# Optimization experiments

Hardware: AMD Instinct MI355X
Metric: run time of the kernel (lower is better)

## Reference

```python
import jax, jax.numpy as jnp
import numpy as np

D_MODEL = 1024
D_K = 64
B, S = 4, 2048


def setup_inputs() -> dict:
    key = jax.random.key(0)
    k1, k2, k3, k4, k5, k6, k7 = jax.random.split(key, 7)
    return {
        "query": jax.random.normal(k1, (B, S, D_MODEL), dtype=jnp.float32),
        "key": jax.random.normal(k2, (B, S, D_MODEL), dtype=jnp.float32),
        "value": jax.random.normal(k3, (B, S, D_MODEL), dtype=jnp.float32),
        "mask": jax.random.randint(k4, (B, S, S), 0, 2).astype(jnp.bool_),
        # nn.Linear(d_model, d_k, bias=False) weights, stored as [d_k, d_model] like torch
        "w_q": jax.random.normal(k5, (D_K, D_MODEL), dtype=jnp.float32) * (D_MODEL ** -0.5),
        "w_k": jax.random.normal(k6, (D_K, D_MODEL), dtype=jnp.float32) * (D_MODEL ** -0.5),
        "w_v": jax.random.normal(k7, (D_K, D_MODEL), dtype=jnp.float32) * (D_MODEL ** -0.5),
    }


def reference(query, key, value, mask, w_q, w_k, w_v):
    # Linear projections (torch Linear: x @ W.T)
    q = jnp.einsum("bsm,km->bsk", query, w_q)   # [B,S,d_k]
    k = jnp.einsum("bsm,km->bsk", key, w_k)
    v = jnp.einsum("bsm,km->bsk", value, w_v)
    # NOTE: original scales by d_model**-0.5 (not d_k) — keep faithful.
    scores = jnp.einsum("bqk,bsk->bqs", q, k) * (D_MODEL ** -0.5)  # [B,S,S]
    # NOTE: original fills masked positions with 1e-9 (not -inf) BEFORE softmax.
    scores = jnp.where(mask, jnp.float32(1e-9), scores)
    probs = jax.nn.softmax(scores, axis=-1)
    return jnp.einsum("bqs,bsk->bqk", probs, v)  # [B,S,d_k]
```

## Files before the change

kernel.cpp:

```cpp
#include <hip/hip_runtime.h>

#define B_    4
#define S_    2048
#define DM_   1024
#define DK_   64
#define SCALE_ 0.03125f

typedef float        f32x4  __attribute__((ext_vector_type(4)));
typedef float        float8 __attribute__((ext_vector_type(8)));
typedef short        short8 __attribute__((ext_vector_type(8)));
typedef float        fltx4  __attribute__((ext_vector_type(4)));
typedef unsigned int uint2v __attribute__((ext_vector_type(2)));
typedef unsigned int uint4v __attribute__((ext_vector_type(4)));

static __device__ __forceinline__ unsigned short f2bf(float f) {
  unsigned u = __float_as_uint(f);
  u += 0x7fffu + ((u >> 16) & 1u);
  return (unsigned short)(u >> 16);
}
static __device__ __forceinline__ uint2v pack4(float a, float b, float c, float d) {
  uint2v r;
  r.x = (unsigned)f2bf(a) | ((unsigned)f2bf(b) << 16);
  r.y = (unsigned)f2bf(c) | ((unsigned)f2bf(d) << 16);
  return r;
}
static __device__ __forceinline__ short8 cvt8(float8 v) {
  short8 r;
#pragma unroll
  for (int i = 0; i < 8; ++i) r[i] = (short)f2bf(v[i]);
  return r;
}

__global__ void detect_kernel(const unsigned int* __restrict__ m, unsigned int* __restrict__ flag) {
  unsigned v = m[threadIdx.x];
  unsigned long long bad = __ballot(v > 1u);
  if (threadIdx.x == 0) flag[0] = (bad != 0ull) ? 1u : 0u;
}

__global__ __launch_bounds__(256) void wconv_kernel(
    const float* __restrict__ wq, const float* __restrict__ wk, const float* __restrict__ wv,
    unsigned short* __restrict__ Wb)
{
  const int idx   = blockIdx.x * 256 + threadIdx.x;
  const int which = idx >> 13;
  const int e     = idx & 8191;
  const float* __restrict__ w = (which == 0) ? wq : (which == 1) ? wk : wv;
  fltx4 v0 = *reinterpret_cast<const fltx4*>(w + (size_t)e * 8);
  fltx4 v1 = *reinterpret_cast<const fltx4*>(w + (size_t)e * 8 + 4);
  uint4v o;
  o.x = (unsigned)f2bf(v0.x) | ((unsigned)f2bf(v0.y) << 16);
  o.y = (unsigned)f2bf(v0.z) | ((unsigned)f2bf(v0.w) << 16);
  o.z = (unsigned)f2bf(v1.x) | ((unsigned)f2bf(v1.y) << 16);
  o.w = (unsigned)f2bf(v1.z) | ((unsigned)f2bf(v1.w) << 16);
  *reinterpret_cast<uint4v*>(Wb + (size_t)which * 65536 + (size_t)e * 8) = o;
}

__global__ __launch_bounds__(256) void maskpack_kernel(const unsigned char* __restrict__ mb,
                                                       const unsigned int* __restrict__ mi,
                                                       const unsigned int* __restrict__ flag,
                                                       unsigned int* __restrict__ mp) {
  const int w = blockIdx.x * 256 + threadIdx.x;
  unsigned out = 0;
  if (flag[0]) {
    const uint4v* p = reinterpret_cast<const uint4v*>(mb + (size_t)w * 32);
    uint4v a = p[0], b = p[1];
    unsigned ws0[8];
    ws0[0]=a.x; ws0[1]=a.y; ws0[2]=a.z; ws0[3]=a.w; ws0[4]=b.x; ws0[5]=b.y; ws0[6]=b.z; ws0[7]=b.w;
#pragma unroll
    for (int i = 0; i < 8; ++i) {
      unsigned v = ws0[i];
      out |= ((v & 0x000000ffu) ? 1u : 0u) << (i * 4 + 0);
      out |= ((v & 0x0000ff00u) ? 1u : 0u) << (i * 4 + 1);
      out |= ((v & 0x00ff0000u) ? 1u : 0u) << (i * 4 + 2);
      out |= ((v & 0xff000000u) ? 1u : 0u) << (i * 4 + 3);
    }
  } else {
    const uint4v* p = reinterpret_cast<const uint4v*>(mi + (size_t)w * 32);
#pragma unroll
    for (int i = 0; i < 8; ++i) {
      uint4v a = p[i];
      out |= (a.x ? 1u : 0u) << (i * 4 + 0);
      out |= (a.y ? 1u : 0u) << (i * 4 + 1);
      out |= (a.z ? 1u : 0u) << (i * 4 + 2);
      out |= (a.w ? 1u : 0u) << (i * 4 + 3);
    }
  }
  mp[w] = out;
}

__global__ __launch_bounds__(256) void proj3_kernel(
    const float* __restrict__ xq, const float* __restrict__ xk, const float* __restrict__ xv,
    const unsigned short* __restrict__ Wb,
    unsigned short* __restrict__ Qp, unsigned short* __restrict__ Kp, unsigned short* __restrict__ Vt)
{
  const int which = blockIdx.y;
  const float* __restrict__ x = (which == 0) ? xq : (which == 1) ? xk : xv;
  const int row0 = blockIdx.x * 16;
  const int tid = threadIdx.x, wid = tid >> 6, lane = tid & 63;
  const int g = lane >> 4, r16 = lane & 15;

  const float* __restrict__ xrow = x + (size_t)(row0 + r16) * DM_ + wid * 256 + g * 8;
  const unsigned short* __restrict__ wbase = Wb + (size_t)which * 65536 + wid * 256 + g * 8;

  f32x4 acc[4];
#pragma unroll
  for (int i = 0; i < 4; ++i) { acc[i].x = 0.f; acc[i].y = 0.f; acc[i].z = 0.f; acc[i].w = 0.f; }

#pragma unroll
  for (int kc = 0; kc < 8; ++kc) {
    float8 xa = *reinterpret_cast<const float8*>(xrow + kc * 32);
    short8 w0 = *reinterpret_cast<const short8*>(wbase + (size_t)(0 * 16 + r16) * DM_ + kc * 32);
    short8 w1 = *reinterpret_cast<const short8*>(wbase + (size_t)(1 * 16 + r16) * DM_ + kc * 32);
    short8 w2 = *reinterpret_cast<const short8*>(wbase + (size_t)(2 * 16 + r16) * DM_ + kc * 32);
    short8 w3 = *reinterpret_cast<const short8*>(wbase + (size_t)(3 * 16 + r16) * DM_ + kc * 32);
    short8 a = cvt8(xa);
    acc[0] = __builtin_amdgcn_mfma_f32_16x16x32_bf16(a, w0, acc[0], 0, 0, 0);
    acc[1] = __builtin_amdgcn_mfma_f32_16x16x32_bf16(a, w1, acc[1], 0, 0, 0);
    acc[2] = __builtin_amdgcn_mfma_f32_16x16x32_bf16(a, w2, acc[2], 0, 0, 0);
    acc[3] = __builtin_amdgcn_mfma_f32_16x16x32_bf16(a, w3, acc[3], 0, 0, 0);
  }

  __shared__ f32x4 red[4][4][64];
#pragma unroll
  for (int nf = 0; nf < 4; ++nf) red[wid][nf][lane] = acc[nf];
  __syncthreads();

  f32x4 s = red[0][wid][lane];
#pragma unroll
  for (int w = 1; w < 4; ++w) {
    f32x4 t = red[w][wid][lane];
    s.x += t.x; s.y += t.y; s.z += t.z; s.w += t.w;
  }

  if (which < 2) {
    unsigned short* __restrict__ dst = (which == 0) ? Qp : Kp;
#pragma unroll
    for (int j = 0; j < 4; ++j)
      dst[(size_t)(row0 + g * 4 + j) * DK_ + wid * 16 + r16] = f2bf(s[j]);
  } else {
    const int grow = row0 + g * 4;
    const int bb = grow >> 11, sin = grow & 2047;
    *reinterpret_cast<uint2v*>(Vt + (size_t)(bb * DK_ + wid * 16 + r16) * S_ + sin) =
        pack4(s.x, s.y, s.z, s.w);
  }
}

__global__ __launch_bounds__(64) void attn_part_kernel(
    const unsigned short* __restrict__ Qp, const unsigned short* __restrict__ Kp,
    const unsigned short* __restrict__ Vt, const unsigned int* __restrict__ mp,
    float* __restrict__ pacc, float* __restrict__ pm, float* __restrict__ pl)
{
  const int lane = threadIdx.x;
  const int g = lane >> 4, r16 = lane & 15;
  const int bx = blockIdx.x;
  const int sp = bx >> 9;
  const int qw = bx & 511;
  const int b  = qw >> 7;
  const int q0 = (qw & 127) * 16;

  __shared__ __align__(16) unsigned short Kt[64][72];
  __shared__ __align__(16) unsigned short Vs[64][72];
  __shared__ __align__(16) unsigned short Pq[16][72];

  short8 aq0, aq1;
  {
    const unsigned short* qrow = Qp + (size_t)(b * S_ + q0 + r16) * DK_ + g * 8;
    aq0 = *reinterpret_cast<const short8*>(qrow);
    aq1 = *reinterpret_cast<const short8*>(qrow + 32);
  }

  float mrun[4], lsum[4], corr[4];
  f32x4 acc[4];
#pragma unroll
  for (int j = 0; j < 4; ++j) { mrun[j] = -3.0e38f; lsum[j] = 0.f; }
#pragma unroll
  for (int nf = 0; nf < 4; ++nf) { acc[nf].x = 0.f; acc[nf].y = 0.f; acc[nf].z = 0.f; acc[nf].w = 0.f; }

  const int srow_stage = lane >> 3, sgran = lane & 7;

  for (int st = sp * 8; st < sp * 8 + 8; ++st) {
    const int s0 = st * 64;
#pragma unroll
    for (int i = 0; i < 8; ++i) {
      int r = i * 8 + srow_stage;
      uint4v kv = *reinterpret_cast<const uint4v*>(Kp + (size_t)(b * S_ + s0 + r) * DK_ + sgran * 8);
      *reinterpret_cast<uint4v*>(&Kt[r][sgran * 8]) = kv;
      uint4v vv = *reinterpret_cast<const uint4v*>(Vt + (size_t)(b * DK_ + r) * S_ + s0 + sgran * 8);
      *reinterpret_cast<uint4v*>(&Vs[r][sgran * 8]) = vv;
    }
    unsigned long long mw[4];
#pragma unroll
    for (int j = 0; j < 4; ++j) {
      size_t widx = ((size_t)(b * S_ + q0 + g * 4 + j) * S_ + s0) >> 5;
      mw[j] = *reinterpret_cast<const unsigned long long*>(mp + widx);
    }
    __syncthreads();

    f32x4 sc[4];
#pragma unroll
    for (int nf = 0; nf < 4; ++nf) { sc[nf].x = 0.f; sc[nf].y = 0.f; sc[nf].z = 0.f; sc[nf].w = 0.f; }
#pragma unroll
    for (int nf = 0; nf < 4; ++nf) {
      short8 bk0 = *reinterpret_cast<const short8*>(&Kt[nf * 16 + r16][g * 8]);
      short8 bk1 = *reinterpret_cast<const short8*>(&Kt[nf * 16 + r16][32 + g * 8]);
      sc[nf] = __builtin_amdgcn_mfma_f32_16x16x32_bf16(aq0, bk0, sc[nf], 0, 0, 0);
      sc[nf] = __builtin_amdgcn_mfma_f32_16x16x32_bf16(aq1, bk1, sc[nf], 0, 0, 0);
    }
#pragma unroll
    for (int nf = 0; nf < 4; ++nf)
#pragma unroll
      for (int j = 0; j < 4; ++j) {
        float v = sc[nf][j] * SCALE_;
        sc[nf][j] = ((mw[j] >> (nf * 16 + r16)) & 1ull) ? 1e-9f : v;
      }
#pragma unroll
    for (int j = 0; j < 4; ++j) {
      float tm = fmaxf(fmaxf(sc[0][j], sc[1][j]), fmaxf(sc[2][j], sc[3][j]));
#pragma unroll
      for (int off = 1; off < 16; off <<= 1) tm = fmaxf(tm, __shfl_xor(tm, off));
      float mn = fmaxf(mrun[j], tm);
      corr[j] = __expf(mrun[j] - mn);
      mrun[j] = mn;
    }
#pragma unroll
    for (int nf = 0; nf < 4; ++nf)
#pragma unroll
      for (int j = 0; j < 4; ++j)
        sc[nf][j] = __expf(sc[nf][j] - mrun[j]);
#pragma unroll
    for (int j = 0; j < 4; ++j) {
      float rs = (sc[0][j] + sc[1][j]) + (sc[2][j] + sc[3][j]);
#pragma unroll
      for (int off = 1; off < 16; off <<= 1) rs += __shfl_xor(rs, off);
      lsum[j] = lsum[j] * corr[j] + rs;
    }
#pragma unroll
    for (int nf = 0; nf < 4; ++nf) {
      acc[nf].x *= corr[0]; acc[nf].y *= corr[1]; acc[nf].z *= corr[2]; acc[nf].w *= corr[3];
    }
#pragma unroll
    for (int nf = 0; nf < 4; ++nf)
#pragma unroll
      for (int j = 0; j < 4; ++j)
        Pq[g * 4 + j][nf * 16 + r16] = f2bf(sc[nf][j]);
    asm volatile("s_waitcnt lgkmcnt(0)" ::: "memory");

#pragma unroll
    for (int k2 = 0; k2 < 2; ++k2) {
      short8 pa = *reinterpret_cast<const short8*>(&Pq[r16][k2 * 32 + g * 8]);
#pragma unroll
      for (int nf = 0; nf < 4; ++nf) {
        short8 bv = *reinterpret_cast<const short8*>(&Vs[nf * 16 + r16][k2 * 32 + g * 8]);
        acc[nf] = __builtin_amdgcn_mfma_f32_16x16x32_bf16(pa, bv, acc[nf], 0, 0, 0);
      }
    }
    __syncthreads();
  }

  float* __restrict__ pa = pacc + (size_t)(sp * 512 + qw) * 1024;
#pragma unroll
  for (int nf = 0; nf < 4; ++nf)
#pragma unroll
    for (int j = 0; j < 4; ++j)
      pa[(g * 4 + j) * 64 + nf * 16 + r16] = acc[nf][j];
  if (r16 == 0) {
#pragma unroll
    for (int j = 0; j < 4; ++j) {
      pm[(sp * 512 + qw) * 16 + g * 4 + j] = mrun[j];
      pl[(sp * 512 + qw) * 16 + g * 4 + j] = lsum[j];
    }
  }
}

__global__ __launch_bounds__(64) void attn_merge_kernel(
    const float* __restrict__ pacc, const float* __restrict__ pm, const float* __restrict__ pl,
    float* __restrict__ out)
{
  const int qw = blockIdx.x;
  const int b = qw >> 7, q0 = (qw & 127) * 16;
  const int lane = threadIdx.x;

#pragma unroll 1
  for (int row = 0; row < 16; ++row) {
    float m0 = pm[(0 * 512 + qw) * 16 + row], m1 = pm[(1 * 512 + qw) * 16 + row];
    float m2 = pm[(2 * 512 + qw) * 16 + row], m3 = pm[(3 * 512 + qw) * 16 + row];
    float M = fmaxf(fmaxf(m0, m1), fmaxf(m2, m3));
    float w0 = __expf(m0 - M), w1 = __expf(m1 - M), w2 = __expf(m2 - M), w3 = __expf(m3 - M);
    float L = w0 * pl[(0 * 512 + qw) * 16 + row] + w1 * pl[(1 * 512 + qw) * 16 + row] +
              w2 * pl[(2 * 512 + qw) * 16 + row] + w3 * pl[(3 * 512 + qw) * 16 + row];
    float v = w0 * pacc[((size_t)(0 * 512 + qw) * 16 + row) * 64 + lane] +
              w1 * pacc[((size_t)(1 * 512 + qw) * 16 + row) * 64 + lane] +
              w2 * pacc[((size_t)(2 * 512 + qw) * 16 + row) * 64 + lane] +
              w3 * pacc[((size_t)(3 * 512 + qw) * 16 + row) * 64 + lane];
    out[(size_t)(b * S_ + q0 + row) * DK_ + lane] = v / L;
  }
}

__global__ __launch_bounds__(64) void attn_kernel(
    const unsigned short* __restrict__ Qp, const unsigned short* __restrict__ Kp,
    const unsigned short* __restrict__ Vt, const unsigned int* __restrict__ mp,
    float* __restrict__ out)
{
  const int lane = threadIdx.x;
  const int g = lane >> 4, r16 = lane & 15;
  const int qt = blockIdx.x & 127;
  const int b  = blockIdx.x >> 7;
  const int q0 = qt * 16;

  __shared__ __align__(16) unsigned short Kt[64][72];
  __shared__ __align__(16) unsigned short Vs[64][72];
  __shared__ __align__(16) unsigned short Pq[16][72];

  short8 aq0, aq1;
  {
    const unsigned short* qrow = Qp + (size_t)(b * S_ + q0 + r16) * DK_ + g * 8;
    aq0 = *reinterpret_cast<const short8*>(qrow);
    aq1 = *reinterpret_cast<const short8*>(qrow + 32);
  }

  float mrun[4], lsum[4], corr[4];
  f32x4 acc[4];
#pragma unroll
  for (int j = 0; j < 4; ++j) { mrun[j] = -3.0e38f; lsum[j] = 0.f; }
#pragma unroll
  for (int nf = 0; nf < 4; ++nf) { acc[nf].x = 0.f; acc[nf].y = 0.f; acc[nf].z = 0.f; acc[nf].w = 0.f; }

  const int srow_stage = lane >> 3, sgran = lane & 7;

  for (int st = 0; st < 32; ++st) {
    const int s0 = st * 64;
#pragma unroll
    for (int i = 0; i < 8; ++i) {
      int r = i * 8 + srow_stage;
      uint4v kv = *reinterpret_cast<const uint4v*>(Kp + (size_t)(b * S_ + s0 + r) * DK_ + sgran * 8);
      *reinterpret_cast<uint4v*>(&Kt[r][sgran * 8]) = kv;
      uint4v vv = *reinterpret_cast<const uint4v*>(Vt + (size_t)(b * DK_ + r) * S_ + s0 + sgran * 8);
      *reinterpret_cast<uint4v*>(&Vs[r][sgran * 8]) = vv;
    }
    unsigned long long mw[4];
#pragma unroll
    for (int j = 0; j < 4; ++j) {
      size_t widx = ((size_t)(b * S_ + q0 + g * 4 + j) * S_ + s0) >> 5;
      mw[j] = *reinterpret_cast<const unsigned long long*>(mp + widx);
    }
    __syncthreads();

    f32x4 sc[4];
#pragma unroll
    for (int nf = 0; nf < 4; ++nf) { sc[nf].x = 0.f; sc[nf].y = 0.f; sc[nf].z = 0.f; sc[nf].w = 0.f; }
#pragma unroll
    for (int nf = 0; nf < 4; ++nf) {
      short8 bk0 = *reinterpret_cast<const short8*>(&Kt[nf * 16 + r16][g * 8]);
      short8 bk1 = *reinterpret_cast<const short8*>(&Kt[nf * 16 + r16][32 + g * 8]);
      sc[nf] = __builtin_amdgcn_mfma_f32_16x16x32_bf16(aq0, bk0, sc[nf], 0, 0, 0);
      sc[nf] = __builtin_amdgcn_mfma_f32_16x16x32_bf16(aq1, bk1, sc[nf], 0, 0, 0);
    }
#pragma unroll
    for (int nf = 0; nf < 4; ++nf)
#pragma unroll
      for (int j = 0; j < 4; ++j) {
        float v = sc[nf][j] * SCALE_;
        sc[nf][j] = ((mw[j] >> (nf * 16 + r16)) & 1ull) ? 1e-9f : v;
      }
#pragma unroll
    for (int j = 0; j < 4; ++j) {
      float tm = fmaxf(fmaxf(sc[0][j], sc[1][j]), fmaxf(sc[2][j], sc[3][j]));
#pragma unroll
      for (int off = 1; off < 16; off <<= 1) tm = fmaxf(tm, __shfl_xor(tm, off));
      float mn = fmaxf(mrun[j], tm);
      corr[j] = __expf(mrun[j] - mn);
      mrun[j] = mn;
    }
#pragma unroll
    for (int nf = 0; nf < 4; ++nf)
#pragma unroll
      for (int j = 0; j < 4; ++j)
        sc[nf][j] = __expf(sc[nf][j] - mrun[j]);
#pragma unroll
    for (int j = 0; j < 4; ++j) {
      float rs = (sc[0][j] + sc[1][j]) + (sc[2][j] + sc[3][j]);
#pragma unroll
      for (int off = 1; off < 16; off <<= 1) rs += __shfl_xor(rs, off);
      lsum[j] = lsum[j] * corr[j] + rs;
    }
#pragma unroll
    for (int nf = 0; nf < 4; ++nf) {
      acc[nf].x *= corr[0]; acc[nf].y *= corr[1]; acc[nf].z *= corr[2]; acc[nf].w *= corr[3];
    }
#pragma unroll
    for (int nf = 0; nf < 4; ++nf)
#pragma unroll
      for (int j = 0; j < 4; ++j)
        Pq[g * 4 + j][nf * 16 + r16] = f2bf(sc[nf][j]);
    asm volatile("s_waitcnt lgkmcnt(0)" ::: "memory");

#pragma unroll
    for (int k2 = 0; k2 < 2; ++k2) {
      short8 pa = *reinterpret_cast<const short8*>(&Pq[r16][k2 * 32 + g * 8]);
#pragma unroll
      for (int nf = 0; nf < 4; ++nf) {
        short8 bv = *reinterpret_cast<const short8*>(&Vs[nf * 16 + r16][k2 * 32 + g * 8]);
        acc[nf] = __builtin_amdgcn_mfma_f32_16x16x32_bf16(pa, bv, acc[nf], 0, 0, 0);
      }
    }
    __syncthreads();
  }

#pragma unroll
  for (int nf = 0; nf < 4; ++nf)
#pragma unroll
    for (int j = 0; j < 4; ++j)
      out[(size_t)(b * S_ + q0 + g * 4 + j) * DK_ + nf * 16 + r16] = acc[nf][j] / lsum[j];
}

extern "C" void kernel_launch(void* const* d_in, const int* in_sizes, int n_in,
                              void* d_out, int out_size, void* d_ws, size_t ws_size,
                              hipStream_t stream) {
  const float* q  = (const float*)d_in[0];
  const float* k  = (const float*)d_in[1];
  const float* v  = (const float*)d_in[2];
  const void*  mk = d_in[3];
  const float* wq = (const float*)d_in[4];
  const float* wk = (const float*)d_in[5];
  const float* wv = (const float*)d_in[6];

  char* ws = (char*)d_ws;
  unsigned short* Qp   = (unsigned short*)(ws);
  unsigned short* Kp   = (unsigned short*)(ws + (1u << 20));
  unsigned short* Vt   = (unsigned short*)(ws + (2u << 20));
  unsigned int*   mp   = (unsigned int*)  (ws + (3u << 20));
  unsigned int*   flag = (unsigned int*)  (ws + (5u << 20));
  unsigned short* Wb   = (unsigned short*)(ws + (5u << 20) + 4096);
  float*          pacc = (float*)(ws + (6u << 20));
  float*          pm   = (float*)(ws + (14u << 20));
  float*          pl   = (float*)(ws + (14u << 20) + (1u << 17));

  wconv_kernel<<<96, 256, 0, stream>>>(wq, wk, wv, Wb);
  detect_kernel<<<1, 64, 0, stream>>>((const unsigned int*)mk, flag);
  maskpack_kernel<<<2048, 256, 0, stream>>>((const unsigned char*)mk, (const unsigned int*)mk, flag, mp);
  proj3_kernel<<<dim3(512, 3), 256, 0, stream>>>(q, k, v, Wb, Qp, Kp, Vt);

  if (ws_size >= (15u << 20)) {
    attn_part_kernel<<<2048, 64, 0, stream>>>(Qp, Kp, Vt, mp, pacc, pm, pl);
    attn_merge_kernel<<<512, 64, 0, stream>>>(pacc, pm, pl, (float*)d_out);
  } else {
    attn_kernel<<<512, 64, 0, stream>>>(Qp, Kp, Vt, mp, (float*)d_out);
  }
}
```

Measured before the change: 98.61 us.

## Restructure projection kernel with 64-row tiles staged in LDS via direct global loads

The projection kernel now processes 64 rows per block instead of 16. X and weight tiles are loaded with global_load_lds into XOR-swizzled shared memory, and each wave owns 16 rows across the full K dimension, which removes the cross-wave split-K reduction. Each weight tile is now reused across four times more rows, but there are 4x fewer blocks (384) and two syncs per K step with no double buffering, so load latency is not overlapped.

Result: faster. 86.96 us (-11.8%).

```diff
diff --git a/kernel.cpp b/kernel.cpp
--- a/kernel.cpp
+++ b/kernel.cpp
@@ -13,6 +13,11 @@
 typedef unsigned int uint2v __attribute__((ext_vector_type(2)));
 typedef unsigned int uint4v __attribute__((ext_vector_type(4)));
 
+#define GLL16(gsrc, ldst)                                                   \
+  __builtin_amdgcn_global_load_lds(                                         \
+      (const __attribute__((address_space(1))) void*)(gsrc),                \
+      (__attribute__((address_space(3))) void*)(ldst), 16, 0, 0)
+
 static __device__ __forceinline__ unsigned short f2bf(float f) {
   unsigned u = __float_as_uint(f);
   u += 0x7fffu + ((u >> 16) & 1u);
@@ -22,12 +27,6 @@
   uint2v r;
   r.x = (unsigned)f2bf(a) | ((unsigned)f2bf(b) << 16);
   r.y = (unsigned)f2bf(c) | ((unsigned)f2bf(d) << 16);
-  return r;
-}
-static __device__ __forceinline__ short8 cvt8(float8 v) {
-  short8 r;
-#pragma unroll
-  for (int i = 0; i < 8; ++i) r[i] = (short)f2bf(v[i]);
   return r;
 }
 
@@ -88,60 +87,91 @@
   mp[w] = out;
 }
 
-__global__ __launch_bounds__(256) void proj3_kernel(
+__global__ __launch_bounds__(256) void proj4_kernel(
     const float* __restrict__ xq, const float* __restrict__ xk, const float* __restrict__ xv,
     const unsigned short* __restrict__ Wb,
     unsigned short* __restrict__ Qp, unsigned short* __restrict__ Kp, unsigned short* __restrict__ Vt)
 {
   const int which = blockIdx.y;
   const float* __restrict__ x = (which == 0) ? xq : (which == 1) ? xk : xv;
-  const int row0 = blockIdx.x * 16;
-  const int tid = threadIdx.x, wid = tid >> 6, lane = tid & 63;
-  const int g = lane >> 4, r16 = lane & 15;
-
-  const float* __restrict__ xrow = x + (size_t)(row0 + r16) * DM_ + wid * 256 + g * 8;
-  const unsigned short* __restrict__ wbase = Wb + (size_t)which * 65536 + wid * 256 + g * 8;
+  const unsigned short* __restrict__ wsrc = Wb + (size_t)which * 65536;
+  const int row0 = blockIdx.x * 64;
+  const int tid = threadIdx.x, wid = tid >> 6;
+  const int lane = tid & 63, g = lane >> 4, r16 = lane & 15;
+
+  __shared__ __align__(16) float          XsF[8192];
+  __shared__ __align__(16) unsigned short WsH[8192];
 
   f32x4 acc[4];
 #pragma unroll
   for (int i = 0; i < 4; ++i) { acc[i].x = 0.f; acc[i].y = 0.f; acc[i].z = 0.f; acc[i].w = 0.f; }
 
-#pragma unroll
-  for (int kc = 0; kc < 8; ++kc) {
-    float8 xa = *reinterpret_cast<const float8*>(xrow + kc * 32);
-    short8 w0 = *reinterpret_cast<const short8*>(wbase + (size_t)(0 * 16 + r16) * DM_ + kc * 32);
-    short8 w1 = *reinterpret_cast<const short8*>(wbase + (size_t)(1 * 16 + r16) * DM_ + kc * 32);
-    short8 w2 = *reinterpret_cast<const short8*>(wbase + (size_t)(2 * 16 + r16) * DM_ + kc * 32);
-    short8 w3 = *reinterpret_cast<const short8*>(wbase + (size_t)(3 * 16 + r16) * DM_ + kc * 32);
-    short8 a = cvt8(xa);
-    acc[0] = __builtin_amdgcn_mfma_f32_16x16x32_bf16(a, w0, acc[0], 0, 0, 0);
-    acc[1] = __builtin_amdgcn_mfma_f32_16x16x32_bf16(a, w1, acc[1], 0, 0, 0);
-    acc[2] = __builtin_amdgcn_mfma_f32_16x16x32_bf16(a, w2, acc[2], 0, 0, 0);
-    acc[3] = __builtin_amdgcn_mfma_f32_16x16x32_bf16(a, w3, acc[3], 0, 0, 0);
-  }
-
-  __shared__ f32x4 red[4][4][64];
-#pragma unroll
-  for (int nf = 0; nf < 4; ++nf) red[wid][nf][lane] = acc[nf];
-  __syncthreads();
-
-  f32x4 s = red[0][wid][lane];
-#pragma unroll
-  for (int w = 1; w < 4; ++w) {
-    f32x4 t = red[w][wid][lane];
-    s.x += t.x; s.y += t.y; s.z += t.z; s.w += t.w;
+  int xrow[8], xcol[8];
+#pragma unroll
+  for (int i = 0; i < 8; ++i) {
+    int L = i * 4096 + tid * 16;
+    int U = L ^ (((L >> 9) & 15) << 4);
+    xrow[i] = U >> 9;
+    xcol[i] = (U & 511) >> 2;
+  }
+  int wrow[4], wcol[4];
+#pragma unroll
+  for (int i = 0; i < 4; ++i) {
+    int L = i * 4096 + tid * 16;
+    int U = L ^ (((L >> 8) & 15) << 4);
+    wrow[i] = U >> 8;
+    wcol[i] = (U & 255) >> 1;
+  }
+
+  for (int kb = 0; kb < 8; ++kb) {
+    const int k0 = kb * 128;
+#pragma unroll
+    for (int i = 0; i < 8; ++i)
+      GLL16(x + (size_t)(row0 + xrow[i]) * DM_ + k0 + xcol[i],
+            (char*)XsF + i * 4096 + wid * 1024);
+#pragma unroll
+    for (int i = 0; i < 4; ++i)
+      GLL16(wsrc + (size_t)wrow[i] * DM_ + k0 + wcol[i],
+            (char*)WsH + i * 4096 + wid * 1024);
+    __syncthreads();
+
+#pragma unroll
+    for (int k2 = 0; k2 < 4; ++k2) {
+      const int la  = (wid * 16 + r16) * 512 + k2 * 128 + g * 32;
+      const int pa0 = la ^ (r16 << 4);
+      const int pa1 = (la + 16) ^ (r16 << 4);
+      fltx4 a0 = *reinterpret_cast<const fltx4*>((const char*)XsF + pa0);
+      fltx4 a1 = *reinterpret_cast<const fltx4*>((const char*)XsF + pa1);
+      short8 a;
+      a[0] = (short)f2bf(a0.x); a[1] = (short)f2bf(a0.y);
+      a[2] = (short)f2bf(a0.z); a[3] = (short)f2bf(a0.w);
+      a[4] = (short)f2bf(a1.x); a[5] = (short)f2bf(a1.y);
+      a[6] = (short)f2bf(a1.z); a[7] = (short)f2bf(a1.w);
+#pragma unroll
+      for (int nf = 0; nf < 4; ++nf) {
+        const int lb = (nf * 16 + r16) * 256 + k2 * 64 + g * 16;
+        const int pb = lb ^ (r16 << 4);
+        short8 b = *reinterpret_cast<const short8*>((const char*)WsH + pb);
+        acc[nf] = __builtin_amdgcn_mfma_f32_16x16x32_bf16(a, b, acc[nf], 0, 0, 0);
+      }
+    }
+    __syncthreads();
   }
 
   if (which < 2) {
     unsigned short* __restrict__ dst = (which == 0) ? Qp : Kp;
 #pragma unroll
-    for (int j = 0; j < 4; ++j)
-      dst[(size_t)(row0 + g * 4 + j) * DK_ + wid * 16 + r16] = f2bf(s[j]);
+    for (int nf = 0; nf < 4; ++nf)
+#pragma unroll
+      for (int j = 0; j < 4; ++j)
+        dst[(size_t)(row0 + wid * 16 + g * 4 + j) * DK_ + nf * 16 + r16] = f2bf(acc[nf][j]);
   } else {
-    const int grow = row0 + g * 4;
+    const int grow = row0 + wid * 16 + g * 4;
     const int bb = grow >> 11, sin = grow & 2047;
-    *reinterpret_cast<uint2v*>(Vt + (size_t)(bb * DK_ + wid * 16 + r16) * S_ + sin) =
-        pack4(s.x, s.y, s.z, s.w);
+#pragma unroll
+    for (int nf = 0; nf < 4; ++nf)
+      *reinterpret_cast<uint2v*>(Vt + (size_t)(bb * DK_ + nf * 16 + r16) * S_ + sin) =
+          pack4(acc[nf][0], acc[nf][1], acc[nf][2], acc[nf][3]);
   }
 }
 
@@ -438,7 +468,7 @@
   wconv_kernel<<<96, 256, 0, stream>>>(wq, wk, wv, Wb);
   detect_kernel<<<1, 64, 0, stream>>>((const unsigned int*)mk, flag);
   maskpack_kernel<<<2048, 256, 0, stream>>>((const unsigned char*)mk, (const unsigned int*)mk, flag, mp);
-  proj3_kernel<<<dim3(512, 3), 256, 0, stream>>>(q, k, v, Wb, Qp, Kp, Vt);
+  proj4_kernel<<<dim3(128, 3), 256, 0, stream>>>(q, k, v, Wb, Qp, Kp, Vt);
 
   if (ws_size >= (15u << 20)) {
     attn_part_kernel<<<2048, 64, 0, stream>>>(Qp, Kp, Vt, mp, pacc, pm, pl);
```

## Stage projection input rows in LDS as bf16 and split waves over output columns

Applied to the files above, without the earlier changes.

The projection kernel now loads each block's 16 input rows with coalesced float4 reads, converts them to bf16, and stores them in a 32 KB XOR-swizzled LDS tile. Each wave then computes one 16-column slice of the output over the full K dimension from LDS, so the cross-wave LDS reduction is gone. The aim is better global-load coalescing and no reduction step. The cost is a large LDS footprint that may limit occupancy, plus a longer serial chain of 32 MFMAs per wave.

New measurement: 96.01 us. 1.03x faster.

```diff
diff --git a/kernel.cpp b/kernel.cpp
--- a/kernel.cpp
+++ b/kernel.cpp
@@ -7,7 +7,6 @@
 #define SCALE_ 0.03125f
 
 typedef float        f32x4  __attribute__((ext_vector_type(4)));
-typedef float        float8 __attribute__((ext_vector_type(8)));
 typedef short        short8 __attribute__((ext_vector_type(8)));
 typedef float        fltx4  __attribute__((ext_vector_type(4)));
 typedef unsigned int uint2v __attribute__((ext_vector_type(2)));
@@ -22,12 +21,6 @@
   uint2v r;
   r.x = (unsigned)f2bf(a) | ((unsigned)f2bf(b) << 16);
   r.y = (unsigned)f2bf(c) | ((unsigned)f2bf(d) << 16);
-  return r;
-}
-static __device__ __forceinline__ short8 cvt8(float8 v) {
-  short8 r;
-#pragma unroll
-  for (int i = 0; i < 8; ++i) r[i] = (short)f2bf(v[i]);
   return r;
 }
 
@@ -88,7 +81,7 @@
   mp[w] = out;
 }
 
-__global__ __launch_bounds__(256) void proj3_kernel(
+__global__ __launch_bounds__(256) void proj12_kernel(
     const float* __restrict__ xq, const float* __restrict__ xk, const float* __restrict__ xv,
     const unsigned short* __restrict__ Wb,
     unsigned short* __restrict__ Qp, unsigned short* __restrict__ Kp, unsigned short* __restrict__ Vt)
@@ -96,52 +89,46 @@
   const int which = blockIdx.y;
   const float* __restrict__ x = (which == 0) ? xq : (which == 1) ? xk : xv;
   const int row0 = blockIdx.x * 16;
-  const int tid = threadIdx.x, wid = tid >> 6, lane = tid & 63;
-  const int g = lane >> 4, r16 = lane & 15;
-
-  const float* __restrict__ xrow = x + (size_t)(row0 + r16) * DM_ + wid * 256 + g * 8;
-  const unsigned short* __restrict__ wbase = Wb + (size_t)which * 65536 + wid * 256 + g * 8;
-
-  f32x4 acc[4];
-#pragma unroll
-  for (int i = 0; i < 4; ++i) { acc[i].x = 0.f; acc[i].y = 0.f; acc[i].z = 0.f; acc[i].w = 0.f; }
-
-#pragma unroll
-  for (int kc = 0; kc < 8; ++kc) {
-    float8 xa = *reinterpret_cast<const float8*>(xrow + kc * 32);
-    short8 w0 = *reinterpret_cast<const short8*>(wbase + (size_t)(0 * 16 + r16) * DM_ + kc * 32);
-    short8 w1 = *reinterpret_cast<const short8*>(wbase + (size_t)(1 * 16 + r16) * DM_ + kc * 32);
-    short8 w2 = *reinterpret_cast<const short8*>(wbase + (size_t)(2 * 16 + r16) * DM_ + kc * 32);
-    short8 w3 = *reinterpret_cast<const short8*>(wbase + (size_t)(3 * 16 + r16) * DM_ + kc * 32);
-    short8 a = cvt8(xa);
-    acc[0] = __builtin_amdgcn_mfma_f32_16x16x32_bf16(a, w0, acc[0], 0, 0, 0);
-    acc[1] = __builtin_amdgcn_mfma_f32_16x16x32_bf16(a, w1, acc[1], 0, 0, 0);
-    acc[2] = __builtin_amdgcn_mfma_f32_16x16x32_bf16(a, w2, acc[2], 0, 0, 0);
-    acc[3] = __builtin_amdgcn_mfma_f32_16x16x32_bf16(a, w3, acc[3], 0, 0, 0);
-  }
-
-  __shared__ f32x4 red[4][4][64];
-#pragma unroll
-  for (int nf = 0; nf < 4; ++nf) red[wid][nf][lane] = acc[nf];
+  const int tid = threadIdx.x, wid = tid >> 6;
+  const int lane = tid & 63, g = lane >> 4, r16 = lane & 15;
+
+  __shared__ __align__(16) unsigned short Xb[16 * 1024];
+
+  const float* __restrict__ chunk = x + (size_t)(row0 + 4 * wid) * DM_;
+  fltx4 xa[16];
+#pragma unroll
+  for (int i = 0; i < 16; ++i)
+    xa[i] = *reinterpret_cast<const fltx4*>(chunk + i * 256 + lane * 4);
+#pragma unroll
+  for (int i = 0; i < 16; ++i) {
+    const int lrow = 4 * wid + (i >> 2);
+    const int cb   = (i & 3) * 512 + lane * 8;
+    const int addr = lrow * 2048 + (cb ^ ((lrow & 15) << 4));
+    *reinterpret_cast<uint2v*>((char*)Xb + addr) = pack4(xa[i].x, xa[i].y, xa[i].z, xa[i].w);
+  }
   __syncthreads();
 
-  f32x4 s = red[0][wid][lane];
-#pragma unroll
-  for (int w = 1; w < 4; ++w) {
-    f32x4 t = red[w][wid][lane];
-    s.x += t.x; s.y += t.y; s.z += t.z; s.w += t.w;
+  f32x4 acc; acc.x = 0.f; acc.y = 0.f; acc.z = 0.f; acc.w = 0.f;
+  const unsigned short* __restrict__ wb =
+      Wb + (size_t)which * 65536 + (size_t)(wid * 16 + r16) * DM_ + g * 8;
+#pragma unroll
+  for (int kc = 0; kc < 32; ++kc) {
+    const int ra = r16 * 2048 + ((kc * 64 + g * 16) ^ ((r16 & 15) << 4));
+    short8 a = *reinterpret_cast<const short8*>((const char*)Xb + ra);
+    short8 w = *reinterpret_cast<const short8*>(wb + kc * 32);
+    acc = __builtin_amdgcn_mfma_f32_16x16x32_bf16(a, w, acc, 0, 0, 0);
   }
 
   if (which < 2) {
     unsigned short* __restrict__ dst = (which == 0) ? Qp : Kp;
 #pragma unroll
     for (int j = 0; j < 4; ++j)
-      dst[(size_t)(row0 + g * 4 + j) * DK_ + wid * 16 + r16] = f2bf(s[j]);
+      dst[(size_t)(row0 + g * 4 + j) * DK_ + wid * 16 + r16] = f2bf(acc[j]);
   } else {
     const int grow = row0 + g * 4;
     const int bb = grow >> 11, sin = grow & 2047;
     *reinterpret_cast<uint2v*>(Vt + (size_t)(bb * DK_ + wid * 16 + r16) * S_ + sin) =
-        pack4(s.x, s.y, s.z, s.w);
+        pack4(acc.x, acc.y, acc.z, acc.w);
   }
 }
 
@@ -438,7 +425,7 @@
   wconv_kernel<<<96, 256, 0, stream>>>(wq, wk, wv, Wb);
   detect_kernel<<<1, 64, 0, stream>>>((const unsigned int*)mk, flag);
   maskpack_kernel<<<2048, 256, 0, stream>>>((const unsigned char*)mk, (const unsigned int*)mk, flag, mp);
-  proj3_kernel<<<dim3(512, 3), 256, 0, stream>>>(q, k, v, Wb, Qp, Kp, Vt);
+  proj12_kernel<<<dim3(512, 3), 256, 0, stream>>>(q, k, v, Wb, Qp, Kp, Vt);
 
   if (ws_size >= (15u << 20)) {
     attn_part_kernel<<<2048, 64, 0, stream>>>(Qp, Kp, Vt, mp, pacc, pm, pl);
```
